# Kernel optimization log

Hardware: AMD Instinct MI355X
Metric: run time of the kernel (lower is better)

Reference implementation:

```python
import jax, jax.numpy as jnp
import numpy as np

B, C1, C2, K, S, HDIM = 8, 16, 16, 3, 1, 16
H = W = 64


def setup_inputs() -> dict:
    key = jax.random.key(0)
    k0, k1, k2 = jax.random.split(key, 3)
    x = jax.random.normal(k0, (B, C1, H, W), jnp.float32)
    # torch.nn.Linear default init scale ~ 1/sqrt(fan_in)
    fc1_w = jax.random.normal(k1, (HDIM, 5), jnp.float32) * (1.0 / np.sqrt(5.0))
    fc1_b = jnp.zeros((HDIM,), jnp.float32)
    fc2_w = jax.random.normal(k2, (C2 * C1 * K * K, HDIM), jnp.float32) * (1.0 / np.sqrt(HDIM))
    fc2_b = jnp.zeros((C2 * C1 * K * K,), jnp.float32)
    return {"x": x, "fc1_w": fc1_w, "fc1_b": fc1_b, "fc2_w": fc2_w, "fc2_b": fc2_b}


def _unfold_same(x, k, s):
    """F.pad('same'-style) + F.unfold. Returns (patches [B, L, C*k*k], out_h, out_w).
    Channel ordering matches torch unfold: index = c*k*k + i*k + j (channel-major)."""
    Bq, C, Hq, Wq = x.shape
    out_h = (Hq + s - 1) // s
    out_w = (Wq + s - 1) // s
    pad_h = max((out_h - 1) * s + k - Hq, 0)
    pad_w = max((out_w - 1) * s + k - Wq, 0)
    pt, pb = pad_h // 2, pad_h - pad_h // 2
    pl, pr = pad_w // 2, pad_w - pad_w // 2
    xp = jnp.pad(x, ((0, 0), (0, 0), (pt, pb), (pl, pr)))
    # k*k shifted views; loop over tiny fixed k*k=9 taps only
    cols = jnp.stack(
        [xp[:, :, i:i + out_h * s:s, j:j + out_w * s:s] for i in range(k) for j in range(k)],
        axis=2,
    )  # [B, C, k*k, out_h, out_w]
    patches = cols.reshape(Bq, C * k * k, out_h * out_w).transpose(0, 2, 1)  # [B, L, C*k*k]
    return patches, out_h, out_w


def reference(x, fc1_w, fc1_b, fc2_w, fc2_b):
    patches, oh, ow = _unfold_same(x, K, S)  # [B, L, N] with N = C1*K*K
    Bq, L, N = patches.shape
    mu = patches.mean(-1, keepdims=True)
    # torch.std default is unbiased (ddof=1)
    var = jnp.sum((patches - mu) ** 2, axis=-1, keepdims=True) / (N - 1)
    sigma = jnp.sqrt(var) + 1e-6
    normed = (patches - mu) / sigma
    skew = jnp.mean(normed ** 3, axis=-1, keepdims=True)
    kurt = jnp.mean(normed ** 4, axis=-1, keepdims=True) - 3.0
    prob = jax.nn.softmax(patches, axis=-1)
    entropy = -jnp.sum(prob * jnp.log(prob + 1e-6), axis=-1, keepdims=True)
    stats = jnp.concatenate([mu, sigma, skew, kurt, entropy], axis=-1)  # [B, L, 5]
    stats = jax.lax.stop_gradient(stats)  # .detach() in the original
    h = jax.nn.relu(stats @ fc1_w.T + fc1_b)                 # [B, L, hdim]
    weights = (h @ fc2_w.T + fc2_b).reshape(Bq, L, C2, N)    # [B, L, c2, c1*k*k]
    out = jnp.einsum('blco,blo->blc', weights, patches)      # per-location dynamic conv
    return out.transpose(0, 2, 1).reshape(Bq, C2, oh, ow)
```

## Files before the change

### kernel.cpp

```cpp
#include <hip/hip_runtime.h>
#include <math.h>


typedef __attribute__((ext_vector_type(8))) short short8;
typedef __attribute__((ext_vector_type(4))) float float4v;

#define NPq 144

__device__ __forceinline__ unsigned short f2bf(float f) {
    unsigned int u = __builtin_bit_cast(unsigned int, f);
    u += 0x7fffu + ((u >> 16) & 1u);
    return (unsigned short)(u >> 16);
}
__device__ __forceinline__ float bf2f(unsigned short h) {
    unsigned int u = ((unsigned int)h) << 16;
    return __builtin_bit_cast(float, u);
}

__global__ void prep_bfrag(const float* __restrict__ fc2_w,
                           const float* __restrict__ fc2_b,
                           unsigned short* __restrict__ Bfrag) {
    const int blk  = blockIdx.x;
    const int t    = blk / 5, s = blk % 5;
    const int lane = threadIdx.x;
    const int n    = lane & 15, q = lane >> 4;
    short8 v;
#pragma unroll
    for (int j = 0; j < 8; ++j) {
        const int k = s * 32 + q * 8 + j;
        float w = 0.f;
        if (k < NPq) w = (t < 16) ? fc2_w[(t * NPq + k) * 16 + n]
                                  : fc2_b[n * NPq + k];
        v[j] = (short)f2bf(w);
    }
    *(short8*)(Bfrag + (size_t)(blk * 64 + lane) * 8) = v;
}

__global__ __launch_bounds__(256, 2) void sacconv_kernel(
    const float* __restrict__ x,
    const float* __restrict__ fc1_w,
    const float* __restrict__ fc1_b,
    const unsigned short* __restrict__ Bfrag,
    float* __restrict__ out)
{
    __shared__ unsigned short SA[4 * 5 * 64 * 8];
    __shared__ unsigned short Qs[64 * 280];
    __shared__ float Hl[64][20];

    const int t   = threadIdx.x;
    const int blk = blockIdx.x;
    const int b   = blk >> 6;
    const int y   = blk & 63;

    const int lane = t & 63;
    const int w    = __builtin_amdgcn_readfirstlane(t >> 6);
    const int m    = lane & 15;
    const int q    = lane >> 4;
    const int loc  = w * 16 + m;

    float v[5][8];
    short8 af[5];
    float sum = 0.f, mx = -1e30f;
#pragma unroll
    for (int s = 0; s < 5; ++s) {
#pragma unroll
        for (int j = 0; j < 8; ++j) {
            const int o = s * 32 + q * 8 + j;
            float val = 0.f;
            if (o < NPq) {
                const int c1 = o / 9;
                const int rm = o - c1 * 9;
                const int ii = rm / 3;
                const int jj = rm - ii * 3;
                const int yy = y + ii - 1;
                const int xp = loc + jj - 1;
                if (yy >= 0 && yy < 64 && xp >= 0 && xp < 64)
                    val = x[((b * 16 + c1) * 64 + yy) * 64 + xp];
                sum += val;
                mx = fmaxf(mx, val);
            }
            v[s][j] = val;
            af[s][j] = (short)f2bf(val);
        }
    }
    sum += __shfl_xor(sum, 16, 64);
    sum += __shfl_xor(sum, 32, 64);
    mx = fmaxf(mx, __shfl_xor(mx, 16, 64));
    mx = fmaxf(mx, __shfl_xor(mx, 32, 64));
    const float mu = sum * (1.f / 144.f);

    float m2 = 0.f, m3 = 0.f, m4 = 0.f, se = 0.f, sev = 0.f;
#pragma unroll
    for (int s = 0; s < 5; ++s) {
#pragma unroll
        for (int j = 0; j < 8; ++j) {
            const int o = s * 32 + q * 8 + j;
            if (o < NPq) {
                const float d  = v[s][j] - mu;
                const float d2 = d * d;
                m2 += d2; m3 += d2 * d; m4 += d2 * d2;
                const float e = __expf(v[s][j] - mx);
                se += e; sev += e * v[s][j];
            }
        }
    }
    m2 += __shfl_xor(m2, 16, 64);  m2 += __shfl_xor(m2, 32, 64);
    m3 += __shfl_xor(m3, 16, 64);  m3 += __shfl_xor(m3, 32, 64);
    m4 += __shfl_xor(m4, 16, 64);  m4 += __shfl_xor(m4, 32, 64);
    se += __shfl_xor(se, 16, 64);  se += __shfl_xor(se, 32, 64);
    sev += __shfl_xor(sev, 16, 64); sev += __shfl_xor(sev, 32, 64);

    const float var   = m2 * (1.f / 143.f);
    const float sigma = sqrtf(var) + 1e-6f;
    const float is    = 1.f / sigma;
    const float is2   = is * is;
    const float skew  = (m3 * (1.f / 144.f)) * is2 * is;
    const float kurt  = (m4 * (1.f / 144.f)) * is2 * is2 - 3.f;
    const float ent   = __logf(se) + mx - sev / se;

    {
        float h4[4];
#pragma unroll
        for (int j0 = 0; j0 < 4; ++j0) {
            const int j = q * 4 + j0;
            const float* wr = fc1_w + j * 5;
            const float hv = mu * wr[0] + sigma * wr[1] + skew * wr[2]
                           + kurt * wr[3] + ent * wr[4] + fc1_b[j];
            h4[j0] = fmaxf(hv, 0.f);
        }
        *(float4*)&Hl[loc][q * 4] = make_float4(h4[0], h4[1], h4[2], h4[3]);
    }

#pragma unroll
    for (int s = 0; s < 5; ++s)
        *(short8*)&SA[((w * 5 + s) * 64 + lane) * 8] = af[s];

    __syncthreads();

    const int mp = w >> 1;
    const int nh = w & 1;
    const int nb = nh * 8;

    short8 af2[2][5];
#pragma unroll
    for (int mm = 0; mm < 2; ++mm)
#pragma unroll
        for (int s = 0; s < 5; ++s)
            af2[mm][s] = *(const short8*)&SA[(((2 * mp + mm) * 5 + s) * 64 + lane) * 8];

    float4v acc[18];
#pragma unroll
    for (int i = 0; i < 18; ++i) acc[i] = (float4v){0.f, 0.f, 0.f, 0.f};

    const short8* Bf = (const short8*)Bfrag;
    short8 bcur[5], bnxt[5];
#pragma unroll
    for (int s = 0; s < 5; ++s) bcur[s] = Bf[(nb * 5 + s) * 64 + lane];

#pragma unroll
    for (int u = 0; u < 9; ++u) {
        if (u < 8) {
#pragma unroll
            for (int s = 0; s < 5; ++s) bnxt[s] = Bf[((nb + u + 1) * 5 + s) * 64 + lane];
        }
#pragma unroll
        for (int mm = 0; mm < 2; ++mm)
#pragma unroll
            for (int s = 0; s < 5; ++s)
                acc[u * 2 + mm] = __builtin_amdgcn_mfma_f32_16x16x32_bf16(
                    af2[mm][s], bcur[s], acc[u * 2 + mm], 0, 0, 0);
        if (u < 8) {
#pragma unroll
            for (int s = 0; s < 5; ++s) bcur[s] = bnxt[s];
        }
    }

    {
        const int nn = lane & 15, qq = lane >> 4;
#pragma unroll
        for (int u = 0; u < 9; ++u) {
            const int col = (nb + u) * 16 + nn;
#pragma unroll
            for (int mm = 0; mm < 2; ++mm) {
                const int rowb = (2 * mp + mm) * 16 + qq * 4;
#pragma unroll
                for (int r = 0; r < 4; ++r)
                    Qs[(rowb + r) * 280 + col] = f2bf(acc[u * 2 + mm][r]);
            }
        }
    }
    __syncthreads();

    {
        float hv[16];
#pragma unroll
        for (int j = 0; j < 16; ++j) hv[j] = Hl[lane][j];
        const int cg = w * 4;
#pragma unroll
        for (int cc = 0; cc < 4; ++cc) {
            const int c = cg + cc;
            const unsigned short* qr = &Qs[lane * 280 + c * 16];
            short8 q0 = *(const short8*)qr;
            short8 q1 = *(const short8*)(qr + 8);
            float res = bf2f(Qs[lane * 280 + 256 + c]);
#pragma unroll
            for (int j = 0; j < 8; ++j) res += hv[j]     * bf2f((unsigned short)q0[j]);
#pragma unroll
            for (int j = 0; j < 8; ++j) res += hv[8 + j] * bf2f((unsigned short)q1[j]);
            out[(b * 16 + c) * 4096 + y * 64 + lane] = res;
        }
    }
}

extern "C" void kernel_launch(void* const* d_in, const int* in_sizes, int n_in,
                              void* d_out, int out_size, void* d_ws, size_t ws_size,
                              hipStream_t stream) {
    const float* x     = (const float*)d_in[0];
    const float* fc1_w = (const float*)d_in[1];
    const float* fc1_b = (const float*)d_in[2];
    const float* fc2_w = (const float*)d_in[3];
    const float* fc2_b = (const float*)d_in[4];
    float* out = (float*)d_out;
    unsigned short* Bfrag = (unsigned short*)d_ws;

    prep_bfrag<<<85, 64, 0, stream>>>(fc2_w, fc2_b, Bfrag);
    sacconv_kernel<<<512, 256, 0, stream>>>(x, fc1_w, fc1_b, Bfrag, out);
}
```

Before: 75.40 us.

## Coalesce patch loads, prefetch B fragments early, repartition MFMA work across waves

Each lane now loads 4 contiguous channels times 9 taps instead of a scattered k-indexed set, and the bf16 values are repacked into the MFMA A-fragment layout in shared memory. The B-fragment global loads are issued before and during the statistics phase so they overlap the patch loads. The GEMM is redistributed so every wave covers all 4 row tiles and a strided set of output-column tiles, with wave 3 handling the bias tile. The Qs shared-memory row stride is padded to 296 to reduce bank conflicts. The cost is more register pressure from holding 15 B fragments and 20 A fragments, and an imbalanced extra tile on one wave.

New measurement: 72.16 us. 1.04x faster.

```diff
diff --git a/kernel.cpp b/kernel.cpp
--- a/kernel.cpp
+++ b/kernel.cpp
@@ -6,6 +6,7 @@
 typedef __attribute__((ext_vector_type(4))) float float4v;
 
 #define NPq 144
+#define QSTR 296
 
 __device__ __forceinline__ unsigned short f2bf(float f) {
     unsigned int u = __builtin_bit_cast(unsigned int, f);
@@ -44,7 +45,7 @@
     float* __restrict__ out)
 {
     __shared__ unsigned short SA[4 * 5 * 64 * 8];
-    __shared__ unsigned short Qs[64 * 280];
+    __shared__ unsigned short Qs[64 * QSTR];
     __shared__ float Hl[64][20];
 
     const int t   = threadIdx.x;
@@ -58,31 +59,50 @@
     const int q    = lane >> 4;
     const int loc  = w * 16 + m;
 
-    float v[5][8];
-    short8 af[5];
+    const short8* Bf = (const short8*)Bfrag;
+    short8 bb0[5], bb1[5], bb2[5];
+#pragma unroll
+    for (int s = 0; s < 5; ++s) bb0[s] = Bf[(w * 5 + s) * 64 + lane];
+
+    float v[36];
     float sum = 0.f, mx = -1e30f;
 #pragma unroll
-    for (int s = 0; s < 5; ++s) {
-#pragma unroll
-        for (int j = 0; j < 8; ++j) {
-            const int o = s * 32 + q * 8 + j;
-            float val = 0.f;
-            if (o < NPq) {
-                const int c1 = o / 9;
-                const int rm = o - c1 * 9;
-                const int ii = rm / 3;
-                const int jj = rm - ii * 3;
-                const int yy = y + ii - 1;
-                const int xp = loc + jj - 1;
-                if (yy >= 0 && yy < 64 && xp >= 0 && xp < 64)
-                    val = x[((b * 16 + c1) * 64 + yy) * 64 + xp];
-                sum += val;
-                mx = fmaxf(mx, val);
-            }
-            v[s][j] = val;
-            af[s][j] = (short)f2bf(val);
-        }
-    }
+    for (int i = 0; i < 36; ++i) {
+        const int g  = i / 9;
+        const int r9 = i % 9;
+        const int ii = r9 / 3, jj = r9 % 3;
+        const int yy = y + ii - 1;
+        const int xp = loc + jj - 1;
+        float val = 0.f;
+        if (yy >= 0 && yy < 64 && xp >= 0 && xp < 64)
+            val = x[((b * 16 + 4 * q + g) * 64 + yy) * 64 + xp];
+        v[i] = val;
+        sum += val;
+        mx  = fmaxf(mx, val);
+    }
+
+    {
+        unsigned int pk[18];
+#pragma unroll
+        for (int p = 0; p < 18; ++p)
+            pk[p] = (unsigned int)f2bf(v[2 * p]) | ((unsigned int)f2bf(v[2 * p + 1]) << 16);
+        const int g0 = (36 * q) >> 3;
+        auto hwa = [&](int g) { return ((w * 5 + (g >> 2)) * 64 + (g & 3) * 16 + m) * 8; };
+        if ((q & 1) == 0) {
+#pragma unroll
+            for (int u = 0; u < 4; ++u)
+                *(uint4*)&SA[hwa(g0 + u)] = make_uint4(pk[4*u], pk[4*u+1], pk[4*u+2], pk[4*u+3]);
+            *(uint2*)&SA[hwa(g0 + 4)] = make_uint2(pk[16], pk[17]);
+        } else {
+            *(uint2*)&SA[hwa(g0) + 4] = make_uint2(pk[0], pk[1]);
+#pragma unroll
+            for (int u = 0; u < 4; ++u)
+                *(uint4*)&SA[hwa(g0 + 1 + u)] = make_uint4(pk[4*u+2], pk[4*u+3], pk[4*u+4], pk[4*u+5]);
+        }
+        if (lane < 32)
+            *(uint4*)&SA[((w * 5 + 4) * 64 + 32 + lane) * 8] = make_uint4(0u, 0u, 0u, 0u);
+    }
+
     sum += __shfl_xor(sum, 16, 64);
     sum += __shfl_xor(sum, 32, 64);
     mx = fmaxf(mx, __shfl_xor(mx, 16, 64));
@@ -91,18 +111,12 @@
 
     float m2 = 0.f, m3 = 0.f, m4 = 0.f, se = 0.f, sev = 0.f;
 #pragma unroll
-    for (int s = 0; s < 5; ++s) {
-#pragma unroll
-        for (int j = 0; j < 8; ++j) {
-            const int o = s * 32 + q * 8 + j;
-            if (o < NPq) {
-                const float d  = v[s][j] - mu;
-                const float d2 = d * d;
-                m2 += d2; m3 += d2 * d; m4 += d2 * d2;
-                const float e = __expf(v[s][j] - mx);
-                se += e; sev += e * v[s][j];
-            }
-        }
+    for (int i = 0; i < 36; ++i) {
+        const float d  = v[i] - mu;
+        const float d2 = d * d;
+        m2 += d2; m3 += d2 * d; m4 += d2 * d2;
+        const float e = __expf(v[i] - mx);
+        se += e; sev += e * v[i];
     }
     m2 += __shfl_xor(m2, 16, 64);  m2 += __shfl_xor(m2, 32, 64);
     m3 += __shfl_xor(m3, 16, 64);  m3 += __shfl_xor(m3, 32, 64);
@@ -132,60 +146,86 @@
     }
 
 #pragma unroll
-    for (int s = 0; s < 5; ++s)
-        *(short8*)&SA[((w * 5 + s) * 64 + lane) * 8] = af[s];
+    for (int s = 0; s < 5; ++s) bb1[s] = Bf[((w + 4) * 5 + s) * 64 + lane];
 
     __syncthreads();
 
-    const int mp = w >> 1;
-    const int nh = w & 1;
-    const int nb = nh * 8;
-
-    short8 af2[2][5];
-#pragma unroll
-    for (int mm = 0; mm < 2; ++mm)
-#pragma unroll
-        for (int s = 0; s < 5; ++s)
-            af2[mm][s] = *(const short8*)&SA[(((2 * mp + mm) * 5 + s) * 64 + lane) * 8];
-
-    float4v acc[18];
-#pragma unroll
-    for (int i = 0; i < 18; ++i) acc[i] = (float4v){0.f, 0.f, 0.f, 0.f};
-
-    const short8* Bf = (const short8*)Bfrag;
-    short8 bcur[5], bnxt[5];
-#pragma unroll
-    for (int s = 0; s < 5; ++s) bcur[s] = Bf[(nb * 5 + s) * 64 + lane];
-
-#pragma unroll
-    for (int u = 0; u < 9; ++u) {
-        if (u < 8) {
-#pragma unroll
-            for (int s = 0; s < 5; ++s) bnxt[s] = Bf[((nb + u + 1) * 5 + s) * 64 + lane];
-        }
-#pragma unroll
-        for (int mm = 0; mm < 2; ++mm)
+    short8 af[4][5];
+#pragma unroll
+    for (int mm = 0; mm < 4; ++mm)
+#pragma unroll
+        for (int s = 0; s < 5; ++s)
+            af[mm][s] = *(const short8*)&SA[((mm * 5 + s) * 64 + lane) * 8];
+
+    float4v acc[4][4];
+#pragma unroll
+    for (int u = 0; u < 4; ++u)
+#pragma unroll
+        for (int mm = 0; mm < 4; ++mm) acc[u][mm] = (float4v){0.f, 0.f, 0.f, 0.f};
+    float4v acc4[4];
+#pragma unroll
+    for (int mm = 0; mm < 4; ++mm) acc4[mm] = (float4v){0.f, 0.f, 0.f, 0.f};
+
+#pragma unroll
+    for (int s = 0; s < 5; ++s) bb2[s] = Bf[((w + 8) * 5 + s) * 64 + lane];
+#pragma unroll
+    for (int mm = 0; mm < 4; ++mm)
+#pragma unroll
+        for (int s = 0; s < 5; ++s)
+            acc[0][mm] = __builtin_amdgcn_mfma_f32_16x16x32_bf16(af[mm][s], bb0[s], acc[0][mm], 0, 0, 0);
+
+#pragma unroll
+    for (int s = 0; s < 5; ++s) bb0[s] = Bf[((w + 12) * 5 + s) * 64 + lane];
+#pragma unroll
+    for (int mm = 0; mm < 4; ++mm)
+#pragma unroll
+        for (int s = 0; s < 5; ++s)
+            acc[1][mm] = __builtin_amdgcn_mfma_f32_16x16x32_bf16(af[mm][s], bb1[s], acc[1][mm], 0, 0, 0);
+
+    if (w == 3) {
+#pragma unroll
+        for (int s = 0; s < 5; ++s) bb1[s] = Bf[(16 * 5 + s) * 64 + lane];
+    }
+#pragma unroll
+    for (int mm = 0; mm < 4; ++mm)
+#pragma unroll
+        for (int s = 0; s < 5; ++s)
+            acc[2][mm] = __builtin_amdgcn_mfma_f32_16x16x32_bf16(af[mm][s], bb2[s], acc[2][mm], 0, 0, 0);
+
+#pragma unroll
+    for (int mm = 0; mm < 4; ++mm)
+#pragma unroll
+        for (int s = 0; s < 5; ++s)
+            acc[3][mm] = __builtin_amdgcn_mfma_f32_16x16x32_bf16(af[mm][s], bb0[s], acc[3][mm], 0, 0, 0);
+
+    if (w == 3) {
+#pragma unroll
+        for (int mm = 0; mm < 4; ++mm)
 #pragma unroll
             for (int s = 0; s < 5; ++s)
-                acc[u * 2 + mm] = __builtin_amdgcn_mfma_f32_16x16x32_bf16(
-                    af2[mm][s], bcur[s], acc[u * 2 + mm], 0, 0, 0);
-        if (u < 8) {
-#pragma unroll
-            for (int s = 0; s < 5; ++s) bcur[s] = bnxt[s];
-        }
+                acc4[mm] = __builtin_amdgcn_mfma_f32_16x16x32_bf16(af[mm][s], bb1[s], acc4[mm], 0, 0, 0);
     }
 
     {
         const int nn = lane & 15, qq = lane >> 4;
 #pragma unroll
-        for (int u = 0; u < 9; ++u) {
-            const int col = (nb + u) * 16 + nn;
-#pragma unroll
-            for (int mm = 0; mm < 2; ++mm) {
-                const int rowb = (2 * mp + mm) * 16 + qq * 4;
+        for (int u = 0; u < 4; ++u) {
+            const int col = (w + 4 * u) * 16 + nn;
+#pragma unroll
+            for (int mm = 0; mm < 4; ++mm) {
+                const int rowb = mm * 16 + qq * 4;
 #pragma unroll
                 for (int r = 0; r < 4; ++r)
-                    Qs[(rowb + r) * 280 + col] = f2bf(acc[u * 2 + mm][r]);
+                    Qs[(rowb + r) * QSTR + col] = f2bf(acc[u][mm][r]);
+            }
+        }
+        if (w == 3) {
+#pragma unroll
+            for (int mm = 0; mm < 4; ++mm) {
+                const int rowb = mm * 16 + qq * 4;
+#pragma unroll
+                for (int r = 0; r < 4; ++r)
+                    Qs[(rowb + r) * QSTR + 256 + nn] = f2bf(acc4[mm][r]);
             }
         }
     }
@@ -199,10 +239,10 @@
 #pragma unroll
         for (int cc = 0; cc < 4; ++cc) {
             const int c = cg + cc;
-            const unsigned short* qr = &Qs[lane * 280 + c * 16];
+            const unsigned short* qr = &Qs[lane * QSTR + c * 16];
             short8 q0 = *(const short8*)qr;
             short8 q1 = *(const short8*)(qr + 8);
-            float res = bf2f(Qs[lane * 280 + 256 + c]);
+            float res = bf2f(Qs[lane * QSTR + 256 + c]);
 #pragma unroll
             for (int j = 0; j < 8; ++j) res += hv[j]     * bf2f((unsigned short)q0[j]);
 #pragma unroll
```
